# Performance work log

Measured on AMD Instinct MI355X. Metric: run time of the kernel, lower is better.

The kernel has to match this reference:

```python
import jax, jax.numpy as jnp
import numpy as np

B, S, D = 8, 2048, 512
EPS = float(jnp.finfo(jnp.float32).eps)  # torch RMSNorm eps=None -> finfo eps


def rmsnorm(x, w):
    var = jnp.mean(jnp.square(x), axis=-1, keepdims=True)
    return x * jax.lax.rsqrt(var + EPS) * w


def setup_inputs() -> dict:
    key = jax.random.key(0)
    ks = jax.random.split(key, 9)
    x = jax.random.normal(ks[0], (B, S, D), dtype=jnp.float32)
    q_expl = jax.random.normal(ks[1], (B, S, D), dtype=jnp.float32)
    k_expl = jax.random.normal(ks[2], (B, S, D), dtype=jnp.float32)
    # parameters (torch Linear: y = x @ W^T + b; store W already transposed [in, out])
    sc1 = 1.0 / np.sqrt(D)
    W1 = jax.random.uniform(ks[3], (D, 2 * D), jnp.float32, -sc1, sc1)
    b1 = jax.random.uniform(ks[4], (2 * D,), jnp.float32, -sc1, sc1)
    W2 = jax.random.uniform(ks[5], (D, D), jnp.float32, -sc1, sc1)
    b2 = jax.random.uniform(ks[6], (D,), jnp.float32, -sc1, sc1)
    norm1_w = jnp.ones((D,), jnp.float32)
    norm2_w = jnp.ones((D,), jnp.float32)
    return {"x": x, "q_expl": q_expl, "k_expl": k_expl,
            "W1": W1, "b1": b1, "W2": W2, "b2": b2,
            "norm1_w": norm1_w, "norm2_w": norm2_w}


def reference(x, q_expl, k_expl, W1, b1, W2, b2, norm1_w, norm2_w):
    d = x.shape[-1]
    # single-head attention: scores [B,S,S]
    scores = jnp.einsum('bqd,bkd->bqk', q_expl, k_expl) / jnp.sqrt(jnp.float32(d))
    attn = jax.nn.softmax(scores, axis=-1)
    attn_out = jnp.einsum('bqk,bkd->bqd', attn, x)
    # dropout is identity in eval mode
    h = rmsnorm(x + attn_out, norm1_w)
    # GeGLU FFN: Linear(D->2D), chunk, gelu(x1)*x2, Linear(D->D)
    proj = h @ W1 + b1
    x1, x2 = jnp.split(proj, 2, axis=-1)
    g = jax.nn.gelu(x1, approximate=False) * x2
    ff = g @ W2 + b2
    return rmsnorm(h + ff, norm2_w)
```

## Files before the change

### kernel.cpp

```cpp
#include <hip/hip_runtime.h>
#include <math.h>

static constexpr float EPS_F = 1.1920929e-07f;
static constexpr float SCL   = 0.044194173824159216f;

typedef __attribute__((ext_vector_type(8))) short  short8;
typedef __attribute__((ext_vector_type(4))) float  floatx4;

__device__ __forceinline__ float4 ld4(const float* p){ return *(const float4*)p; }
__device__ __forceinline__ ushort f2bf(float f){
  union { float f; unsigned u; } v; v.f = f;
  return (ushort)((v.u + 0x7FFFu + ((v.u >> 16) & 1u)) >> 16);
}
__device__ __forceinline__ float bf2f(ushort h){
  union { unsigned u; float f; } v; v.u = ((unsigned)h) << 16;
  return v.f;
}
#define MFMA16(A,B,C) __builtin_amdgcn_mfma_f32_16x16x32_bf16((A),(B),(C),0,0,0)

__device__ __forceinline__ void gld16(void* lds, const void* g){
  __builtin_amdgcn_global_load_lds(
      (const __attribute__((address_space(1))) unsigned int*)g,
      (__attribute__((address_space(3))) unsigned int*)lds, 16, 0, 0);
}


__global__ __launch_bounds__(256)
void prep(const float* __restrict__ q, const float* __restrict__ k,
          const float* __restrict__ x, const float* __restrict__ W1,
          const float* __restrict__ W2,
          ushort* __restrict__ Qb, ushort* __restrict__ Kb,
          ushort* __restrict__ XT, ushort* __restrict__ W1T,
          ushort* __restrict__ W2T)
{
  const int bi = blockIdx.x, t = threadIdx.x;
  if (bi < 8192){
    const size_t i4 = ((size_t)bi*256 + t)*4;
    float4 v = ld4(q + i4);
    ushort4 o;
    o.x=f2bf(v.x*SCL); o.y=f2bf(v.y*SCL); o.z=f2bf(v.z*SCL); o.w=f2bf(v.w*SCL);
    *(ushort4*)(Qb + i4) = o;
    float4 u = ld4(k + i4);
    o.x=f2bf(u.x); o.y=f2bf(u.y); o.z=f2bf(u.z); o.w=f2bf(u.w);
    *(ushort4*)(Kb + i4) = o;
    return;
  }
  const float* in; ushort* out; int R, C, c0, r0; size_t boff;
  if (bi < 10240){
    const int id = bi - 8192;
    in = x; out = XT; R = 2048; C = 512;
    boff = (size_t)(id >> 8) * R * C;
    c0 = (id & 7)*64; r0 = ((id >> 3) & 31)*64;
  } else if (bi < 10368){
    const int id = bi - 10240;
    in = W1; out = W1T; R = 512; C = 1024; boff = 0;
    c0 = (id & 15)*64; r0 = (id >> 4)*64;
  } else {
    const int id = bi - 10368;
    in = W2; out = W2T; R = 512; C = 512; boff = 0;
    c0 = (id & 7)*64; r0 = (id >> 3)*64;
  }
  __shared__ __align__(16) ushort tile[64*68];
#pragma unroll
  for (int it = 0; it < 4; ++it){
    int f = t + it*256, r = f >> 4, c4 = f & 15;
    float4 v = ld4(in + boff + (size_t)(r0+r)*C + c0 + c4*4);
    ushort4 o; o.x=f2bf(v.x); o.y=f2bf(v.y); o.z=f2bf(v.z); o.w=f2bf(v.w);
    *(ushort4*)&tile[r*68 + c4*4] = o;
  }
  __syncthreads();
#pragma unroll
  for (int it = 0; it < 4; ++it){
    int f = t + it*256, c = f >> 4, q4 = f & 15;
    ushort4 o;
    o.x = tile[(q4*4+0)*68 + c];
    o.y = tile[(q4*4+1)*68 + c];
    o.z = tile[(q4*4+2)*68 + c];
    o.w = tile[(q4*4+3)*68 + c];
    *(ushort4*)(out + boff + (size_t)(c0+c)*R + r0 + q4*4) = o;
  }
}

__global__ __launch_bounds__(512, 4)
void qk2(const ushort* __restrict__ Qbf, const ushort* __restrict__ Kbf,
         ushort* __restrict__ scores, float* __restrict__ rowsum)
{
  extern __shared__ __align__(16) ushort smem[];
  const int t = threadIdx.x, lane = t & 63, w = t >> 6;
  const int id = blockIdx.x;
  const int b = id & 7, s = id >> 3;
  const int m0 = (s & 7) * 256, n0 = (s >> 3) * 128;
  const ushort* Ab = Qbf + ((size_t)b*2048 + m0)*512;
  const ushort* Bb = Kbf + ((size_t)b*2048 + n0)*512;
  const int wr = w >> 1, wc = w & 1;
  const int l15 = lane & 15, quad = lane >> 4;
  const int rl = ((lane >> 2) & 14) | (((lane >> 2) ^ (lane >> 4)) & 1);
  const int cl = (lane & 3) ^ (rl & 3);
  const int sw = (l15 & 7) * 8;
  int aoff[4], boff[4];
#pragma unroll
  for (int m = 0; m < 4; ++m)
    aoff[m] = ((wr*64 + m*16 + l15)*32 + quad*8) ^ sw;
#pragma unroll
  for (int n = 0; n < 4; ++n)
    boff[n] = ((wc*64 + n*16 + l15)*32 + quad*8) ^ sw;
  const size_t aS0 = (size_t)(w*16 + rl)*512 + cl*8;
  const size_t aS1 = aS0 + (size_t)128*512;
  const size_t bS0 = (size_t)(w*16 + rl)*512 + cl*8;
  const int aD = w*512, bD = 16384 + w*512;

  floatx4 acc[4][4];
#pragma unroll
  for (int i = 0; i < 4; ++i)
#pragma unroll
    for (int j = 0; j < 4; ++j) acc[i][j] = (floatx4){0.f,0.f,0.f,0.f};

  const int NT = 16;
  gld16(smem + aD,        Ab + aS0);
  gld16(smem + 4096 + aD, Ab + aS1);
  gld16(smem + bD,        Bb + bS0);
  gld16(smem + 4096 + bD, Bb + bS0 + 32);
  asm volatile("s_waitcnt vmcnt(1)" ::: "memory");
  __builtin_amdgcn_s_barrier();

  short8 af[2], bfr[4];
  for (int kt = 0; kt < NT; ++kt){
    const int cur = kt & 1;
    const ushort* A  = smem + cur*8192;
    const ushort* Bt = smem + 16384 + cur*4096;
#pragma unroll
    for (int n = 0; n < 4; ++n) bfr[n] = *(const short8*)&Bt[boff[n]];
#pragma unroll
    for (int m = 0; m < 2; ++m) af[m] = *(const short8*)&A[aoff[m]];
    if (kt+1 < NT){
      ushort* d = smem + (cur^1)*8192;
      const size_t ko = (size_t)(kt+1)*32;
      gld16(d + aD,        Ab + aS0 + ko);
      gld16(d + 4096 + aD, Ab + aS1 + ko);
    }
    __builtin_amdgcn_s_barrier();
    asm volatile("s_waitcnt lgkmcnt(0)" ::: "memory");
    __builtin_amdgcn_sched_barrier(0);
    __builtin_amdgcn_s_setprio(1);
#pragma unroll
    for (int m = 0; m < 2; ++m)
#pragma unroll
      for (int n = 0; n < 4; ++n)
        acc[m][n] = MFMA16(af[m], bfr[n], acc[m][n]);
    __builtin_amdgcn_s_setprio(0);
    __builtin_amdgcn_s_barrier();
#pragma unroll
    for (int m = 0; m < 2; ++m) af[m] = *(const short8*)&A[aoff[2+m]];
    if (kt+2 < NT)
      gld16(smem + 16384 + cur*4096 + (bD - 16384),
            Bb + bS0 + (size_t)(kt+2)*32);
    __builtin_amdgcn_s_barrier();
    asm volatile("s_waitcnt lgkmcnt(0)" ::: "memory");
    __builtin_amdgcn_sched_barrier(0);
    __builtin_amdgcn_s_setprio(1);
#pragma unroll
    for (int m = 0; m < 2; ++m)
#pragma unroll
      for (int n = 0; n < 4; ++n)
        acc[2+m][n] = MFMA16(af[m], bfr[n], acc[2+m][n]);
    __builtin_amdgcn_s_setprio(0);
    if (kt + 2 < NT) asm volatile("s_waitcnt vmcnt(1)" ::: "memory");
    else             asm volatile("s_waitcnt vmcnt(0)" ::: "memory");
    __builtin_amdgcn_s_barrier();
  }

  ushort* sb = scores + (size_t)b*2048*2048;
#pragma unroll
  for (int m = 0; m < 4; ++m){
    const int rm = m0 + wr*64 + m*16 + quad*4;
    float rs[4] = {0.f,0.f,0.f,0.f};
#pragma unroll
    for (int n = 0; n < 4; ++n){
      const int cn = n0 + wc*64 + n*16 + l15;
#pragma unroll
      for (int r = 0; r < 4; ++r){
        float e = __expf(acc[m][n][r]);
        ushort eb = f2bf(e);
        sb[(size_t)(rm + r)*2048 + cn] = eb;
        rs[r] += bf2f(eb);
      }
    }
#pragma unroll
    for (int r = 0; r < 4; ++r){
      float p2 = rs[r];
      p2 += __shfl_xor(p2, 1); p2 += __shfl_xor(p2, 2);
      p2 += __shfl_xor(p2, 4); p2 += __shfl_xor(p2, 8);
      if (l15 == 0)
        atomicAdd(&rowsum[(size_t)b*2048 + rm + r], p2);
    }
  }
}

__global__ __launch_bounds__(512)
void pv8(const ushort* __restrict__ P, const ushort* __restrict__ XT,
         const float* __restrict__ rowsum, ushort* __restrict__ attn)
{
  extern __shared__ __align__(16) ushort smem[];
  const int t = threadIdx.x, lane = t & 63, w = t >> 6;
  const int id = blockIdx.x;
  const int b = id & 7, s = id >> 3;
  const int m0 = (s >> 2) * 256;
  const int n0 = (s & 3) * 128;
  const ushort* Pb = P  + ((size_t)b*2048 + m0)*2048;
  const ushort* Xb = XT + ((size_t)b*512  + n0)*2048;
  const int wr = w >> 1, wc = w & 1;
  const int l15 = lane & 15, quad = lane >> 4;
  const int c0  = (quad ^ (l15 & 7)) * 8;
  const int srow = lane >> 3;
  const int skc  = ((lane & 7) ^ srow) * 8;

  floatx4 acc[4][4];
#pragma unroll
  for (int i = 0; i < 4; ++i)
#pragma unroll
    for (int j = 0; j < 4; ++j) acc[i][j] = (floatx4){0.f,0.f,0.f,0.f};

  auto stageA = [&](int buf, int kt, int h){
    ushort* base = smem + buf*24576 + h*8192;
#pragma unroll
    for (int r = 0; r < 2; ++r){
      const int rw = r*8 + w;
      gld16(base + rw*512,
            Pb + (size_t)(h*128 + rw*8 + srow)*2048 + kt*64 + skc);
    }
  };
  auto stageB = [&](int buf, int kt){
    ushort* base = smem + buf*24576 + 16384;
#pragma unroll
    for (int r = 0; r < 2; ++r){
      const int rw = r*8 + w;
      gld16(base + rw*512,
            Xb + (size_t)(rw*8 + srow)*2048 + kt*64 + skc);
    }
  };

  stageA(0, 0, 0);
  stageA(0, 0, 1);
  stageB(0, 0);
  stageB(1, 1);
  asm volatile("s_waitcnt vmcnt(2)" ::: "memory");
  __builtin_amdgcn_s_barrier();

  short8 af[2][2], bfr[4][2];
  const int NT = 32;

  for (int kt = 0; kt < NT; ++kt){
    const int cur = kt & 1;
    const ushort* A  = smem + cur*24576;
    const ushort* Bt = A + 16384;

#pragma unroll
    for (int ni = 0; ni < 4; ++ni)
#pragma unroll
      for (int ks = 0; ks < 2; ++ks)
        bfr[ni][ks] = *(const short8*)
          &Bt[(wc*64 + ni*16 + l15)*64 + (c0 ^ (ks*32))];
#pragma unroll
    for (int mi = 0; mi < 2; ++mi)
#pragma unroll
      for (int ks = 0; ks < 2; ++ks)
        af[mi][ks] = *(const short8*)
          &A[(wr*64 + mi*16 + l15)*64 + (c0 ^ (ks*32))];
    if (kt+1 < NT) stageA(cur^1, kt+1, 0);
    __builtin_amdgcn_s_barrier();
    asm volatile("s_waitcnt lgkmcnt(0)" ::: "memory");
    __builtin_amdgcn_sched_barrier(0);
    __builtin_amdgcn_s_setprio(1);
#pragma unroll
    for (int mi = 0; mi < 2; ++mi)
#pragma unroll
      for (int ni = 0; ni < 4; ++ni)
#pragma unroll
        for (int ks = 0; ks < 2; ++ks)
          acc[mi][ni] = MFMA16(af[mi][ks], bfr[ni][ks], acc[mi][ni]);
    __builtin_amdgcn_s_setprio(0);
    __builtin_amdgcn_s_barrier();

#pragma unroll
    for (int mi = 0; mi < 2; ++mi)
#pragma unroll
      for (int ks = 0; ks < 2; ++ks)
        af[mi][ks] = *(const short8*)
          &A[(wr*64 + (2+mi)*16 + l15)*64 + (c0 ^ (ks*32))];
    if (kt+1 < NT) stageA(cur^1, kt+1, 1);
    if (kt+2 < NT) stageB(cur, kt+2);
    __builtin_amdgcn_s_barrier();
    asm volatile("s_waitcnt lgkmcnt(0)" ::: "memory");
    __builtin_amdgcn_sched_barrier(0);
    __builtin_amdgcn_s_setprio(1);
#pragma unroll
    for (int mi = 0; mi < 2; ++mi)
#pragma unroll
      for (int ni = 0; ni < 4; ++ni)
#pragma unroll
        for (int ks = 0; ks < 2; ++ks)
          acc[2+mi][ni] = MFMA16(af[mi][ks], bfr[ni][ks], acc[2+mi][ni]);
    __builtin_amdgcn_s_setprio(0);
    if (kt + 2 < NT) asm volatile("s_waitcnt vmcnt(2)" ::: "memory");
    else             asm volatile("s_waitcnt vmcnt(0)" ::: "memory");
    __builtin_amdgcn_s_barrier();
  }

  ushort* ab = attn + (size_t)b*2048*512;
#pragma unroll
  for (int m = 0; m < 4; ++m){
    const int rm = m0 + wr*64 + m*16 + quad*4;
    float inv[4];
#pragma unroll
    for (int r = 0; r < 4; ++r)
      inv[r] = 1.0f / rowsum[(size_t)b*2048 + rm + r];
#pragma unroll
    for (int n = 0; n < 4; ++n){
      const int cn = n0 + wc*64 + n*16 + l15;
#pragma unroll
      for (int r = 0; r < 4; ++r)
        ab[(size_t)(rm + r)*512 + cn] = f2bf(acc[m][n][r] * inv[r]);
    }
  }
}

__global__ __launch_bounds__(256)
void res_rms1(const float* __restrict__ x, const float* __restrict__ n1w,
              ushort* __restrict__ ah)
{
  const int wid = threadIdx.x >> 6, lane = threadIdx.x & 63;
  const size_t row = (size_t)blockIdx.x*4 + wid;
  ushort* ar = ah + row*512;
  const float* xr = x + row*512;
  ushort4 a0 = *(const ushort4*)&ar[lane*8];
  ushort4 a1 = *(const ushort4*)&ar[lane*8 + 4];
  float4 x0 = ld4(xr + lane*8), x1 = ld4(xr + lane*8 + 4);
  float h[8];
  h[0]=x0.x+bf2f(a0.x); h[1]=x0.y+bf2f(a0.y); h[2]=x0.z+bf2f(a0.z); h[3]=x0.w+bf2f(a0.w);
  h[4]=x1.x+bf2f(a1.x); h[5]=x1.y+bf2f(a1.y); h[6]=x1.z+bf2f(a1.z); h[7]=x1.w+bf2f(a1.w);
  float ss = 0.f;
#pragma unroll
  for (int e=0;e<8;++e) ss += h[e]*h[e];
#pragma unroll
  for (int s=1;s<64;s<<=1) ss += __shfl_xor(ss, s);
  const float rr = rsqrtf(ss*(1.0f/512.0f) + EPS_F);
  ushort4 o0, o1;
  o0.x=f2bf(h[0]*rr*n1w[lane*8+0]); o0.y=f2bf(h[1]*rr*n1w[lane*8+1]);
  o0.z=f2bf(h[2]*rr*n1w[lane*8+2]); o0.w=f2bf(h[3]*rr*n1w[lane*8+3]);
  o1.x=f2bf(h[4]*rr*n1w[lane*8+4]); o1.y=f2bf(h[5]*rr*n1w[lane*8+5]);
  o1.z=f2bf(h[6]*rr*n1w[lane*8+6]); o1.w=f2bf(h[7]*rr*n1w[lane*8+7]);
  *(ushort4*)&ar[lane*8]     = o0;
  *(ushort4*)&ar[lane*8 + 4] = o1;
}

__global__ __launch_bounds__(512, 4)
void ffn2(const ushort* __restrict__ hbf, const ushort* __restrict__ W1T,
          const float* __restrict__ b1, ushort* __restrict__ gbuf)
{
  extern __shared__ __align__(16) ushort smem[];
  const int t = threadIdx.x, lane = t & 63, w = t >> 6;
  const int id = blockIdx.x;
  const int xcd = id & 7, sl = id >> 3;
  const int m0 = (xcd*8 + (sl >> 3)) * 256;
  const int n0 = (sl & 7) * 64;
  const ushort* Ab = hbf + (size_t)m0*512;
  const int wr = w >> 1, wc = w & 1;
  const int l15 = lane & 15, quad = lane >> 4;
  const int rl = ((lane >> 2) & 14) | (((lane >> 2) ^ (lane >> 4)) & 1);
  const int cl = (lane & 3) ^ (rl & 3);
  const int sw = (l15 & 7) * 8;
  int aoff[4], boff[4];
#pragma unroll
  for (int m = 0; m < 4; ++m)
    aoff[m] = ((wr*64 + m*16 + l15)*32 + quad*8) ^ sw;
#pragma unroll
  for (int n = 0; n < 4; ++n)
    boff[n] = ((wc*64 + n*16 + l15)*32 + quad*8) ^ sw;
  const size_t aS0 = (size_t)(w*16 + rl)*512 + cl*8;
  const size_t aS1 = aS0 + (size_t)128*512;
  const int br = w*16 + rl;
  const int bgrow = ((br >> 5) & 1)*512 + n0 + (br >> 6)*32 + (br & 31);
  const size_t bS0 = (size_t)bgrow*512 + cl*8;
  const int aD = w*512, bD = 16384 + w*512;

  floatx4 acc[4][4];
#pragma unroll
  for (int i = 0; i < 4; ++i)
#pragma unroll
    for (int j = 0; j < 4; ++j) acc[i][j] = (floatx4){0.f,0.f,0.f,0.f};

  const int NT = 16;
  gld16(smem + aD,        Ab + aS0);
  gld16(smem + 4096 + aD, Ab + aS1);
  gld16(smem + bD,        W1T + bS0);
  gld16(smem + 4096 + bD, W1T + bS0 + 32);
  asm volatile("s_waitcnt vmcnt(1)" ::: "memory");
  __builtin_amdgcn_s_barrier();

  short8 af[2], bfr[4];
  for (int kt = 0; kt < NT; ++kt){
    const int cur = kt & 1;
    const ushort* A  = smem + cur*8192;
    const ushort* Bt = smem + 16384 + cur*4096;
#pragma unroll
    for (int n = 0; n < 4; ++n) bfr[n] = *(const short8*)&Bt[boff[n]];
#pragma unroll
    for (int m = 0; m < 2; ++m) af[m] = *(const short8*)&A[aoff[m]];
    if (kt+1 < NT){
      ushort* d = smem + (cur^1)*8192;
      const size_t ko = (size_t)(kt+1)*32;
      gld16(d + aD,        Ab + aS0 + ko);
      gld16(d + 4096 + aD, Ab + aS1 + ko);
    }
    __builtin_amdgcn_s_barrier();
    asm volatile("s_waitcnt lgkmcnt(0)" ::: "memory");
    __builtin_amdgcn_sched_barrier(0);
    __builtin_amdgcn_s_setprio(1);
#pragma unroll
    for (int m = 0; m < 2; ++m)
#pragma unroll
      for (int n = 0; n < 4; ++n)
        acc[m][n] = MFMA16(af[m], bfr[n], acc[m][n]);
    __builtin_amdgcn_s_setprio(0);
    __builtin_amdgcn_s_barrier();
#pragma unroll
    for (int m = 0; m < 2; ++m) af[m] = *(const short8*)&A[aoff[2+m]];
    if (kt+2 < NT)
      gld16(smem + cur*4096 + bD, W1T + bS0 + (size_t)(kt+2)*32);
    __builtin_amdgcn_s_barrier();
    asm volatile("s_waitcnt lgkmcnt(0)" ::: "memory");
    __builtin_amdgcn_sched_barrier(0);
    __builtin_amdgcn_s_setprio(1);
#pragma unroll
    for (int m = 0; m < 2; ++m)
#pragma unroll
      for (int n = 0; n < 4; ++n)
        acc[2+m][n] = MFMA16(af[m], bfr[n], acc[2+m][n]);
    __builtin_amdgcn_s_setprio(0);
    if (kt + 2 < NT) asm volatile("s_waitcnt vmcnt(1)" ::: "memory");
    else             asm volatile("s_waitcnt vmcnt(0)" ::: "memory");
    __builtin_amdgcn_s_barrier();
  }

#pragma unroll
  for (int m = 0; m < 4; ++m){
#pragma unroll
    for (int n = 0; n < 2; ++n){
      const int col = n0 + wc*32 + n*16 + l15;
      const float bb1 = b1[col], bb2 = b1[512 + col];
#pragma unroll
      for (int r = 0; r < 4; ++r){
        const int row = m0 + wr*64 + m*16 + quad*4 + r;
        float x1 = acc[m][n][r]     + bb1;
        float x2 = acc[m][n+2][r]   + bb2;
        float gl = 0.5f*x1*(1.0f + erff(x1*0.70710678118654752f));
        gbuf[(size_t)row*512 + col] = f2bf(gl*x2);
      }
    }
  }
}

__global__ __launch_bounds__(512, 4)
void ff2(const ushort* __restrict__ gb, const ushort* __restrict__ W2T,
         ushort* __restrict__ ff)
{
  extern __shared__ __align__(16) ushort smem[];
  const int t = threadIdx.x, lane = t & 63, w = t >> 6;
  const int id = blockIdx.x;
  const int xcd = id & 7, sl = id >> 3;
  const int m0 = (xcd*8 + (sl >> 2)) * 256;
  const int n0 = (sl & 3) * 128;
  const ushort* Ab = gb  + (size_t)m0*512;
  const ushort* Bb = W2T + (size_t)n0*512;
  const int wr = w >> 1, wc = w & 1;
  const int l15 = lane & 15, quad = lane >> 4;
  const int rl = ((lane >> 2) & 14) | (((lane >> 2) ^ (lane >> 4)) & 1);
  const int cl = (lane & 3) ^ (rl & 3);
  const int sw = (l15 & 7) * 8;
  int aoff[4], boff[4];
#pragma unroll
  for (int m = 0; m < 4; ++m)
    aoff[m] = ((wr*64 + m*16 + l15)*32 + quad*8) ^ sw;
#pragma unroll
  for (int n = 0; n < 4; ++n)
    boff[n] = ((wc*64 + n*16 + l15)*32 + quad*8) ^ sw;
  const size_t aS0 = (size_t)(w*16 + rl)*512 + cl*8;
  const size_t aS1 = aS0 + (size_t)128*512;
  const size_t bS0 = (size_t)(w*16 + rl)*512 + cl*8;
  const int aD = w*512, bD = 16384 + w*512;

  floatx4 acc[4][4];
#pragma unroll
  for (int i = 0; i < 4; ++i)
#pragma unroll
    for (int j = 0; j < 4; ++j) acc[i][j] = (floatx4){0.f,0.f,0.f,0.f};

  const int NT = 16;
  gld16(smem + aD,        Ab + aS0);
  gld16(smem + 4096 + aD, Ab + aS1);
  gld16(smem + bD,        Bb + bS0);
  gld16(smem + 4096 + bD, Bb + bS0 + 32);
  asm volatile("s_waitcnt vmcnt(1)" ::: "memory");
  __builtin_amdgcn_s_barrier();

  short8 af[2], bfr[4];
  for (int kt = 0; kt < NT; ++kt){
    const int cur = kt & 1;
    const ushort* A  = smem + cur*8192;
    const ushort* Bt = smem + 16384 + cur*4096;
#pragma unroll
    for (int n = 0; n < 4; ++n) bfr[n] = *(const short8*)&Bt[boff[n]];
#pragma unroll
    for (int m = 0; m < 2; ++m) af[m] = *(const short8*)&A[aoff[m]];
    if (kt+1 < NT){
      ushort* d = smem + (cur^1)*8192;
      const size_t ko = (size_t)(kt+1)*32;
      gld16(d + aD,        Ab + aS0 + ko);
      gld16(d + 4096 + aD, Ab + aS1 + ko);
    }
    __builtin_amdgcn_s_barrier();
    asm volatile("s_waitcnt lgkmcnt(0)" ::: "memory");
    __builtin_amdgcn_sched_barrier(0);
    __builtin_amdgcn_s_setprio(1);
#pragma unroll
    for (int m = 0; m < 2; ++m)
#pragma unroll
      for (int n = 0; n < 4; ++n)
        acc[m][n] = MFMA16(af[m], bfr[n], acc[m][n]);
    __builtin_amdgcn_s_setprio(0);
    __builtin_amdgcn_s_barrier();
#pragma unroll
    for (int m = 0; m < 2; ++m) af[m] = *(const short8*)&A[aoff[2+m]];
    if (kt+2 < NT)
      gld16(smem + cur*4096 + bD, Bb + bS0 + (size_t)(kt+2)*32);
    __builtin_amdgcn_s_barrier();
    asm volatile("s_waitcnt lgkmcnt(0)" ::: "memory");
    __builtin_amdgcn_sched_barrier(0);
    __builtin_amdgcn_s_setprio(1);
#pragma unroll
    for (int m = 0; m < 2; ++m)
#pragma unroll
      for (int n = 0; n < 4; ++n)
        acc[2+m][n] = MFMA16(af[m], bfr[n], acc[2+m][n]);
    __builtin_amdgcn_s_setprio(0);
    if (kt + 2 < NT) asm volatile("s_waitcnt vmcnt(1)" ::: "memory");
    else             asm volatile("s_waitcnt vmcnt(0)" ::: "memory");
    __builtin_amdgcn_s_barrier();
  }

#pragma unroll
  for (int m = 0; m < 4; ++m){
    const int rm = m0 + wr*64 + m*16 + quad*4;
#pragma unroll
    for (int n = 0; n < 4; ++n){
      const int cn = n0 + wc*64 + n*16 + l15;
#pragma unroll
      for (int r = 0; r < 4; ++r)
        ff[(size_t)(rm + r)*512 + cn] = f2bf(acc[m][n][r]);
    }
  }
}

__global__ __launch_bounds__(256)
void res_rms2(const ushort* __restrict__ hbf, const ushort* __restrict__ ff,
              const float* __restrict__ b2, const float* __restrict__ n2w,
              float* __restrict__ out)
{
  const int wid = threadIdx.x >> 6, lane = threadIdx.x & 63;
  const size_t row = (size_t)blockIdx.x*4 + wid;
  const ushort* hr = hbf + row*512;
  const ushort* fr = ff  + row*512;
  ushort4 h0 = *(const ushort4*)&hr[lane*8];
  ushort4 h1 = *(const ushort4*)&hr[lane*8 + 4];
  ushort4 f0 = *(const ushort4*)&fr[lane*8];
  ushort4 f1 = *(const ushort4*)&fr[lane*8 + 4];
  float4 bb0 = ld4(b2 + lane*8), bb1 = ld4(b2 + lane*8 + 4);
  float y[8];
  y[0]=bf2f(h0.x)+bf2f(f0.x)+bb0.x; y[1]=bf2f(h0.y)+bf2f(f0.y)+bb0.y;
  y[2]=bf2f(h0.z)+bf2f(f0.z)+bb0.z; y[3]=bf2f(h0.w)+bf2f(f0.w)+bb0.w;
  y[4]=bf2f(h1.x)+bf2f(f1.x)+bb1.x; y[5]=bf2f(h1.y)+bf2f(f1.y)+bb1.y;
  y[6]=bf2f(h1.z)+bf2f(f1.z)+bb1.z; y[7]=bf2f(h1.w)+bf2f(f1.w)+bb1.w;
  float ss = 0.f;
#pragma unroll
  for (int e=0;e<8;++e) ss += y[e]*y[e];
#pragma unroll
  for (int s=1;s<64;s<<=1) ss += __shfl_xor(ss, s);
  const float rr = rsqrtf(ss*(1.0f/512.0f) + EPS_F);
  float4 w0 = ld4(n2w + lane*8), w1 = ld4(n2w + lane*8 + 4);
  float* orow = out + row*512;
  float4 o0, o1;
  o0.x=y[0]*rr*w0.x; o0.y=y[1]*rr*w0.y; o0.z=y[2]*rr*w0.z; o0.w=y[3]*rr*w0.w;
  o1.x=y[4]*rr*w1.x; o1.y=y[5]*rr*w1.y; o1.z=y[6]*rr*w1.z; o1.w=y[7]*rr*w1.w;
  *(float4*)(orow + lane*8)     = o0;
  *(float4*)(orow + lane*8 + 4) = o1;
}

extern "C" void kernel_launch(void* const* d_in, const int* in_sizes, int n_in,
                              void* d_out, int out_size, void* d_ws, size_t ws_size,
                              hipStream_t stream)
{
  const float* x   = (const float*)d_in[0];
  const float* q   = (const float*)d_in[1];
  const float* k   = (const float*)d_in[2];
  const float* W1  = (const float*)d_in[3];
  const float* b1  = (const float*)d_in[4];
  const float* W2  = (const float*)d_in[5];
  const float* b2  = (const float*)d_in[6];
  const float* n1w = (const float*)d_in[7];
  const float* n2w = (const float*)d_in[8];
  float* out = (float*)d_out;

  ushort* scoresP = (ushort*)d_ws;
  ushort* XT  = scoresP + (size_t)8*2048*2048;
  ushort* Qbf = XT  + (size_t)8*512*2048;
  ushort* Kbf = Qbf + (size_t)8*2048*512;
  ushort* W1T = Kbf + (size_t)8*2048*512;
  ushort* W2T = W1T + (size_t)1024*512;
  float*  rowsum = (float*)(W2T + (size_t)512*512);
  ushort* attn = Qbf;
  ushort* hbf  = Qbf;
  ushort* gbuf = Kbf;
  ushort* ffb  = scoresP;

  hipMemsetAsync(rowsum, 0, (size_t)8*2048*sizeof(float), stream);
  prep     <<<dim3(10432),  256, 0, stream>>>(q, k, x, W1, W2, Qbf, Kbf, XT, W1T, W2T);
  qk2      <<<dim3(1024),   512, 49152, stream>>>(Qbf, Kbf, scoresP, rowsum);
  pv8      <<<dim3(256),    512, 98304, stream>>>(scoresP, XT, rowsum, attn);
  res_rms1 <<<dim3(4096),   256, 0, stream>>>(x, n1w, hbf);
  ffn2     <<<dim3(512),    512, 49152, stream>>>(hbf, W1T, b1, gbuf);
  ff2      <<<dim3(256),    512, 49152, stream>>>(gbuf, W2T, ffb);
  res_rms2 <<<dim3(4096),   256, 0, stream>>>(hbf, ffb, b2, n2w, out);
}
```

Baseline: 298.0 us.

## Enlarge QK tile to 256x256 and simplify LDS swizzle in GEMM kernels

The QK scores kernel now computes 256x256 output tiles per block instead of 256x128, with 8 waves in a 2x4 layout. Each wave accumulates 8x4 MFMA tiles, and B is double-buffered at full size, raising LDS to 64KB. This halves the grid and cuts redundant global loads of Q and K per output element. The staging and LDS swizzle pattern is also replaced in the QK, FFN1 and FFN2 GEMMs with a simpler row/column mapping meant to reduce bank conflicts, at the cost of more accumulator registers and lower occupancy in the QK kernel.

Result: slower. 577.3 us (+93.8%).

```diff
diff --git a/kernel.cpp b/kernel.cpp
--- a/kernel.cpp
+++ b/kernel.cpp
@@ -82,97 +82,87 @@
 }
 
 __global__ __launch_bounds__(512, 4)
-void qk2(const ushort* __restrict__ Qbf, const ushort* __restrict__ Kbf,
+void qk3(const ushort* __restrict__ Qbf, const ushort* __restrict__ Kbf,
          ushort* __restrict__ scores, float* __restrict__ rowsum)
 {
   extern __shared__ __align__(16) ushort smem[];
   const int t = threadIdx.x, lane = t & 63, w = t >> 6;
   const int id = blockIdx.x;
   const int b = id & 7, s = id >> 3;
-  const int m0 = (s & 7) * 256, n0 = (s >> 3) * 128;
+  const int m0 = (s & 7) * 256, n0 = (s >> 3) * 256;
   const ushort* Ab = Qbf + ((size_t)b*2048 + m0)*512;
   const ushort* Bb = Kbf + ((size_t)b*2048 + n0)*512;
-  const int wr = w >> 1, wc = w & 1;
+  const int wr = w >> 2, wc = w & 3;
   const int l15 = lane & 15, quad = lane >> 4;
-  const int rl = ((lane >> 2) & 14) | (((lane >> 2) ^ (lane >> 4)) & 1);
-  const int cl = (lane & 3) ^ (rl & 3);
-  const int sw = (l15 & 7) * 8;
-  int aoff[4], boff[4];
-#pragma unroll
-  for (int m = 0; m < 4; ++m)
-    aoff[m] = ((wr*64 + m*16 + l15)*32 + quad*8) ^ sw;
-#pragma unroll
-  for (int n = 0; n < 4; ++n)
-    boff[n] = ((wc*64 + n*16 + l15)*32 + quad*8) ^ sw;
-  const size_t aS0 = (size_t)(w*16 + rl)*512 + cl*8;
-  const size_t aS1 = aS0 + (size_t)128*512;
-  const size_t bS0 = (size_t)(w*16 + rl)*512 + cl*8;
-  const int aD = w*512, bD = 16384 + w*512;
-
-  floatx4 acc[4][4];
-#pragma unroll
-  for (int i = 0; i < 4; ++i)
+  const int swk = ((l15 >> 1) & 3) * 8;
+  const int rl  = lane >> 2;
+  const int cl  = (lane & 3) ^ ((lane >> 3) & 3);
+  const int aofb = (wr*128 + l15)*32 + (quad*8 ^ swk);
+  const int bofb = (wc*64  + l15)*32 + (quad*8 ^ swk);
+
+  floatx4 acc[8][4];
+#pragma unroll
+  for (int i = 0; i < 8; ++i)
 #pragma unroll
     for (int j = 0; j < 4; ++j) acc[i][j] = (floatx4){0.f,0.f,0.f,0.f};
 
+  auto stage = [&](int dstE, const ushort* gsrc, int kt){
+#pragma unroll
+    for (int r = 0; r < 2; ++r)
+      gld16(smem + dstE + w*1024 + r*512,
+            gsrc + (size_t)(w*32 + r*16 + rl)*512 + kt*32 + cl*8);
+  };
+
   const int NT = 16;
-  gld16(smem + aD,        Ab + aS0);
-  gld16(smem + 4096 + aD, Ab + aS1);
-  gld16(smem + bD,        Bb + bS0);
-  gld16(smem + 4096 + bD, Bb + bS0 + 32);
-  asm volatile("s_waitcnt vmcnt(1)" ::: "memory");
+  stage(0,             Ab, 0);
+  stage(16384,         Bb, 0);
+  stage(16384 + 8192,  Bb, 1);
+  asm volatile("s_waitcnt vmcnt(2)" ::: "memory");
   __builtin_amdgcn_s_barrier();
 
-  short8 af[2], bfr[4];
+  short8 af[4], bfr[4];
   for (int kt = 0; kt < NT; ++kt){
     const int cur = kt & 1;
     const ushort* A  = smem + cur*8192;
-    const ushort* Bt = smem + 16384 + cur*4096;
-#pragma unroll
-    for (int n = 0; n < 4; ++n) bfr[n] = *(const short8*)&Bt[boff[n]];
-#pragma unroll
-    for (int m = 0; m < 2; ++m) af[m] = *(const short8*)&A[aoff[m]];
-    if (kt+1 < NT){
-      ushort* d = smem + (cur^1)*8192;
-      const size_t ko = (size_t)(kt+1)*32;
-      gld16(d + aD,        Ab + aS0 + ko);
-      gld16(d + 4096 + aD, Ab + aS1 + ko);
-    }
-    __builtin_amdgcn_s_barrier();
-    asm volatile("s_waitcnt lgkmcnt(0)" ::: "memory");
-    __builtin_amdgcn_sched_barrier(0);
-    __builtin_amdgcn_s_setprio(1);
-#pragma unroll
-    for (int m = 0; m < 2; ++m)
+    const ushort* Bt = smem + 16384 + cur*8192;
+#pragma unroll
+    for (int n = 0; n < 4; ++n) bfr[n] = *(const short8*)&Bt[bofb + n*512];
+#pragma unroll
+    for (int m = 0; m < 4; ++m) af[m]  = *(const short8*)&A[aofb + m*512];
+    if (kt+1 < NT) stage((cur^1)*8192, Ab, kt+1);
+    __builtin_amdgcn_s_barrier();
+    asm volatile("s_waitcnt lgkmcnt(0)" ::: "memory");
+    __builtin_amdgcn_sched_barrier(0);
+    __builtin_amdgcn_s_setprio(1);
+#pragma unroll
+    for (int m = 0; m < 4; ++m)
 #pragma unroll
       for (int n = 0; n < 4; ++n)
         acc[m][n] = MFMA16(af[m], bfr[n], acc[m][n]);
     __builtin_amdgcn_s_setprio(0);
     __builtin_amdgcn_s_barrier();
 #pragma unroll
-    for (int m = 0; m < 2; ++m) af[m] = *(const short8*)&A[aoff[2+m]];
-    if (kt+2 < NT)
-      gld16(smem + 16384 + cur*4096 + (bD - 16384),
-            Bb + bS0 + (size_t)(kt+2)*32);
-    __builtin_amdgcn_s_barrier();
-    asm volatile("s_waitcnt lgkmcnt(0)" ::: "memory");
-    __builtin_amdgcn_sched_barrier(0);
-    __builtin_amdgcn_s_setprio(1);
-#pragma unroll
-    for (int m = 0; m < 2; ++m)
+    for (int m = 0; m < 4; ++m) af[m] = *(const short8*)&A[aofb + (4+m)*512];
+    if (kt+2 < NT) stage(16384 + cur*8192, Bb, kt+2);
+    __builtin_amdgcn_s_barrier();
+    asm volatile("s_waitcnt lgkmcnt(0)" ::: "memory");
+    __builtin_amdgcn_sched_barrier(0);
+    __builtin_amdgcn_s_setprio(1);
+#pragma unroll
+    for (int m = 0; m < 4; ++m)
 #pragma unroll
       for (int n = 0; n < 4; ++n)
-        acc[2+m][n] = MFMA16(af[m], bfr[n], acc[2+m][n]);
-    __builtin_amdgcn_s_setprio(0);
-    if (kt + 2 < NT) asm volatile("s_waitcnt vmcnt(1)" ::: "memory");
+        acc[4+m][n] = MFMA16(af[m], bfr[n], acc[4+m][n]);
+    __builtin_amdgcn_s_setprio(0);
+    if (kt + 2 < NT) asm volatile("s_waitcnt vmcnt(2)" ::: "memory");
     else             asm volatile("s_waitcnt vmcnt(0)" ::: "memory");
     __builtin_amdgcn_s_barrier();
   }
 
   ushort* sb = scores + (size_t)b*2048*2048;
 #pragma unroll
-  for (int m = 0; m < 4; ++m){
-    const int rm = m0 + wr*64 + m*16 + quad*4;
+  for (int m = 0; m < 8; ++m){
+    const int rm = m0 + wr*128 + m*16 + quad*4;
     float rs[4] = {0.f,0.f,0.f,0.f};
 #pragma unroll
     for (int n = 0; n < 4; ++n){
@@ -366,9 +356,9 @@
   const ushort* Ab = hbf + (size_t)m0*512;
   const int wr = w >> 1, wc = w & 1;
   const int l15 = lane & 15, quad = lane >> 4;
-  const int rl = ((lane >> 2) & 14) | (((lane >> 2) ^ (lane >> 4)) & 1);
-  const int cl = (lane & 3) ^ (rl & 3);
-  const int sw = (l15 & 7) * 8;
+  const int rl = lane >> 2;
+  const int cl = (lane & 3) ^ ((lane >> 3) & 3);
+  const int sw = ((l15 >> 1) & 3) * 8;
   int aoff[4], boff[4];
 #pragma unroll
   for (int m = 0; m < 4; ++m)
@@ -474,9 +464,9 @@
   const ushort* Bb = W2T + (size_t)n0*512;
   const int wr = w >> 1, wc = w & 1;
   const int l15 = lane & 15, quad = lane >> 4;
-  const int rl = ((lane >> 2) & 14) | (((lane >> 2) ^ (lane >> 4)) & 1);
-  const int cl = (lane & 3) ^ (rl & 3);
-  const int sw = (l15 & 7) * 8;
+  const int rl = lane >> 2;
+  const int cl = (lane & 3) ^ ((lane >> 3) & 3);
+  const int sw = ((l15 >> 1) & 3) * 8;
   int aoff[4], boff[4];
 #pragma unroll
   for (int m = 0; m < 4; ++m)
@@ -624,7 +614,7 @@
 
   hipMemsetAsync(rowsum, 0, (size_t)8*2048*sizeof(float), stream);
   prep     <<<dim3(10432),  256, 0, stream>>>(q, k, x, W1, W2, Qbf, Kbf, XT, W1T, W2T);
-  qk2      <<<dim3(1024),   512, 49152, stream>>>(Qbf, Kbf, scoresP, rowsum);
+  qk3      <<<dim3(512),    512, 65536, stream>>>(Qbf, Kbf, scoresP, rowsum);
   pv8      <<<dim3(256),    512, 98304, stream>>>(scoresP, XT, rowsum, attn);
   res_rms1 <<<dim3(4096),   256, 0, stream>>>(x, n1w, hbf);
   ffn2     <<<dim3(512),    512, 49152, stream>>>(hbf, W1T, b1, gbuf);
```
